# Performance work log

Hardware: AMD Instinct MI355X
Metric: run time of the kernel (lower is better)

The kernel has to match this reference:

```python
import jax, jax.numpy as jnp
import numpy as np

N, C, T, V = 32, 96, 256, 25
S, REL, OUT, BC, KS = 3, 12, 96, 24, 5
DILS = (1, 2)


def setup_inputs() -> dict:
    key = jax.random.key(0)
    ks = jax.random.split(key, 32)
    rn = lambda i, sh, s=1.0: jax.random.normal(ks[i], sh, dtype=jnp.float32) * s
    ru = lambda i, sh: jax.random.uniform(ks[i], sh, dtype=jnp.float32, minval=0.5, maxval=1.5)
    return dict(
        x=rn(0, (N, C, T, V)),
        spd_A=rn(1, (V, V), 0.1),
        A3=rn(2, (S, V, V), 0.1),
        A6=rn(3, (6, V, V), 0.1),
        alpha=jnp.array([0.5], jnp.float32),
        beta=jnp.array([0.5], jnp.float32),
        gamma=jnp.array([0.5], jnp.float32),
        c1_w=rn(4, (S, REL, C), 0.1), c1_b=rn(5, (S, REL), 0.1),
        c2_w=rn(6, (S, REL, C), 0.1), c2_b=rn(7, (S, REL), 0.1),
        c4_w=rn(8, (S, OUT, REL), 0.1), c4_b=rn(9, (S, OUT), 0.1),
        c3_w=rn(10, (S, OUT, C), 0.1), c3_b=rn(11, (S, OUT), 0.1),
        gbn_s=ru(12, (OUT,)), gbn_b=rn(13, (OUT,), 0.1),
        pw_w=rn(14, (4, BC, OUT), 0.1), pw_b=rn(15, (4, BC), 0.1),
        pwbn_s=ru(16, (4, BC)), pwbn_b=rn(17, (4, BC), 0.1),
        tc_w=rn(18, (2, BC, BC, KS), 0.1), tc_b=rn(19, (2, BC), 0.1),
        tcbn_s=ru(20, (2, BC)), tcbn_b=rn(21, (2, BC), 0.1),
        mpbn_s=ru(22, (BC,)), mpbn_b=rn(23, (BC,), 0.1),
    )


def _bn4(h, s, b):  # eval-mode BN folded to per-channel scale/shift, h: [N,C,T,V]
    return h * s[None, :, None, None] + b[None, :, None, None]


def reference(x, spd_A, A3, A6, alpha, beta, gamma,
              c1_w, c1_b, c2_w, c2_b, c4_w, c4_b, c3_w, c3_b,
              gbn_s, gbn_b, pw_w, pw_b, pwbn_s, pwbn_b,
              tc_w, tc_b, tcbn_s, tcbn_b, mpbn_s, mpbn_b):
    # ---- unit_gcn with CTRGC relation modeling ----
    xm = x.mean(axis=2)                                           # [N,C,V] (1x1 conv commutes with T-mean)
    x1 = jnp.einsum('ncv,src->nsrv', xm, c1_w) + c1_b[None, :, :, None]
    x2 = jnp.einsum('ncv,src->nsrv', xm, c2_w) + c2_b[None, :, :, None]
    R = jnp.tanh(x1[..., :, None] - x2[..., None, :])             # [N,S,REL,V,V]
    M = jnp.einsum('nsruv,sor->nsouv', R, c4_w) + c4_b[None, :, :, None, None]
    A6_ex = jnp.tile(A6, (OUT // 6, 1, 1))                        # [OUT,V,V]; A6_ex[c] = A6[c % 6]
    A_at = (M * alpha[0] + A3[None, :, None] + A6_ex[None, None] * beta[0]
            + spd_A * gamma[0])                                   # [N,S,OUT,V,V]
    y = jnp.zeros((N, OUT, T, V), x.dtype)
    for s_ in range(S):
        x3 = jnp.einsum('nctv,oc->notv', x, c3_w[s_]) + c3_b[s_][None, :, None, None]
        y = y + jnp.einsum('nouv,notv->notu', A_at[:, s_], x3)
    y = jax.nn.relu(_bn4(y, gbn_s, gbn_b) + x)                    # residual down = identity (in==out)
    # ---- MultiScale_TemporalConv (internal residual=False) ----
    outs = []
    for b in range(2):  # dilated temporal branches
        h = jax.nn.relu(_bn4(jnp.einsum('nctv,oc->notv', y, pw_w[b])
                             + pw_b[b][None, :, None, None], pwbn_s[b], pwbn_b[b]))
        d = DILS[b]
        pad = 2 * d  # (KS + (KS-1)*(d-1) - 1)//2 for KS=5
        h = jax.lax.conv_general_dilated(
            h, tc_w[b][..., None], window_strides=(1, 1),
            padding=[(pad, pad), (0, 0)], rhs_dilation=(d, 1),
            dimension_numbers=('NCHW', 'OIHW', 'NCHW')) + tc_b[b][None, :, None, None]
        outs.append(_bn4(h, tcbn_s[b], tcbn_b[b]))
    # max-pool branch
    h = jax.nn.relu(_bn4(jnp.einsum('nctv,oc->notv', y, pw_w[2])
                         + pw_b[2][None, :, None, None], pwbn_s[2], pwbn_b[2]))
    h = jax.lax.reduce_window(h, -jnp.inf, jax.lax.max, (1, 1, 3, 1), (1, 1, 1, 1),
                              [(0, 0), (0, 0), (1, 1), (0, 0)])
    outs.append(_bn4(h, mpbn_s, mpbn_b))
    # plain 1x1 branch
    h = jnp.einsum('nctv,oc->notv', y, pw_w[3]) + pw_b[3][None, :, None, None]
    outs.append(_bn4(h, pwbn_s[3], pwbn_b[3]))
    out = jnp.concatenate(outs, axis=1)                           # [N,OUT,T,V]
    return jax.nn.relu(out + x)                                   # outer residual = identity
```

## Files before the change

kernel.cpp:

```cpp
#include <hip/hip_runtime.h>
#include <hip/hip_bf16.h>

typedef __hip_bfloat16 bf16;
typedef __attribute__((ext_vector_type(4))) _Float16 half4;
typedef __attribute__((ext_vector_type(2))) _Float16 half2v;
typedef __attribute__((ext_vector_type(4))) float f32x4;

#define NN 32
#define CC 96
#define TT 256
#define VV 25
#define SS 3
#define RR 12
#define OO 96
#define BCC 24
#define TV (TT*VV)
#define VV2 (VV*VV)

__device__ __forceinline__ float b2f(bf16 v){ return __bfloat162float(v); }
__device__ __forceinline__ bf16  f2b(float v){ return __float2bfloat16(v); }
__device__ __forceinline__ float u2f(unsigned short b){
    union{unsigned u; float f;} a; a.u = ((unsigned)b)<<16; return a.f;
}

__global__ __launch_bounds__(256) void k_mean(const float* __restrict__ x, float* __restrict__ xm)
{
    int idx = blockIdx.x*256 + threadIdx.x;
    if (idx >= NN*CC*VV) return;
    int v  = idx % VV;
    int nc = idx / VV;
    const float* p = x + (size_t)nc*TV + v;
    float s = 0.f;
    for (int t=0;t<TT;t++) s += p[t*VV];
    xm[idx] = s * (1.0f/TT);
}

__global__ __launch_bounds__(256) void k_aat(
    const float* __restrict__ xm,
    const float* __restrict__ c1_w, const float* __restrict__ c1_b,
    const float* __restrict__ c2_w, const float* __restrict__ c2_b,
    const float* __restrict__ c4_w, const float* __restrict__ c4_b,
    const float* __restrict__ A3,  const float* __restrict__ A6, const float* __restrict__ spd,
    const float* __restrict__ alpha, const float* __restrict__ beta, const float* __restrict__ gamma,
    float* __restrict__ Aat)
{
    __shared__ float s_xm[CC*VV];
    __shared__ float s_x1[RR*VV], s_x2[RR*VV];
    __shared__ float s_R[RR*VV2];
    __shared__ float s_c4[OO*RR];
    __shared__ float s_A3[VV2], s_spd[VV2];
    int n = blockIdx.x / SS, s = blockIdx.x % SS;
    int tid = threadIdx.x;
    for (int i=tid;i<CC*VV;i+=256) s_xm[i] = xm[(size_t)n*CC*VV + i];
    for (int i=tid;i<OO*RR;i+=256) s_c4[i] = c4_w[s*OO*RR + i];
    for (int i=tid;i<VV2;i+=256){ s_A3[i]=A3[s*VV2+i]; s_spd[i]=spd[i]; }
    __syncthreads();
    for (int i=tid;i<RR*VV;i+=256){
        int r=i/VV, u=i-r*VV;
        float a1=0.f, a2=0.f;
        for (int c=0;c<CC;c++){
            float xv = s_xm[c*VV+u];
            a1 += c1_w[(s*RR+r)*CC+c]*xv;
            a2 += c2_w[(s*RR+r)*CC+c]*xv;
        }
        s_x1[i]=a1+c1_b[s*RR+r];
        s_x2[i]=a2+c2_b[s*RR+r];
    }
    __syncthreads();
    for (int i=tid;i<RR*VV2;i+=256){
        int r=i/VV2, uv=i-r*VV2, u=uv/VV, v=uv-u*VV;
        s_R[i] = tanhf(s_x1[r*VV+u]-s_x2[r*VV+v]);
    }
    __syncthreads();
    float al=alpha[0], be=beta[0], ga=gamma[0];
    float* op = Aat + ((size_t)n*SS+s)*OO*VV2;
    for (int i=tid;i<OO*VV2;i+=256){
        int o=i/VV2, uv=i-o*VV2;
        float m=0.f;
        #pragma unroll
        for (int r=0;r<RR;r++) m += s_c4[o*RR+r]*s_R[r*VV2+uv];
        m += c4_b[s*OO+o];
        op[i] = m*al + s_A3[uv] + A6[(o%6)*VV2+uv]*be + s_spd[uv]*ga;
    }
}

#define XROW  20
#define X3ROW 84
#define X3OP  (32*X3ROW)
__global__ __launch_bounds__(256,2) void k_gcn(
    const float* __restrict__ x, const float* __restrict__ c3_w, const float* __restrict__ c3_b,
    const float* __restrict__ Aat, const float* __restrict__ gbn_s, const float* __restrict__ gbn_b,
    float* __restrict__ y)
{
    __shared__ __align__(16) _Float16 s_x[800*XROW];
    __shared__ __align__(16) _Float16 s_x3h[4*X3OP];
    __shared__ __align__(16) _Float16 s_w[6*16*16];
    __shared__ float s_cb[16];

    int bi  = blockIdx.x;
    int og  = bi % 24;
    int tcb = (bi/24) & 7;
    int n   = bi / 192;
    int t0  = tcb*32;
    int tid = threadIdx.x;

    for (int i=tid; i<4*32*9; i+=256){
        int op2 = i/288, r2 = i - op2*288;
        int t = r2/9, kk = 75 + (r2 - t*9);
        s_x3h[op2*X3OP + t*X3ROW + kk] = (_Float16)0.f;
    }

    for (int i=tid;i<16*96;i+=256){
        int m=i/96, c=i-m*96;
        float wf = 0.f;
        if (m<12){ int s=m>>2, op=m&3; wf = c3_w[(s*OO + og*4+op)*CC + c]; }
        s_w[((c>>4)*16+m)*16 + (c&15)] = (_Float16)wf;
    }
    if (tid<16){
        float b=0.f;
        if (tid<12){ int s=tid>>2, op=tid&3; b = c3_b[s*OO + og*4+op]; }
        s_cb[tid]=b;
    }

    int l  = tid & 63;
    int li = l & 15, q = l >> 4;
    int wv_id = tid >> 6;
    int o  = og*4 + wv_id;

    half4 areg[2][5];
    #pragma unroll
    for (int mt=0; mt<2; ++mt){
        int u = mt*16 + li;
        #pragma unroll
        for (int kc=0; kc<5; ++kc){
            half4 h;
            #pragma unroll
            for (int e=0; e<4; ++e){
                int k = kc*16 + q*4 + e;
                float av = 0.f;
                if (u < VV && k < 75){
                    int s = k/25, v = k - s*25;
                    av = Aat[(((size_t)n*SS+s)*OO + o)*VV2 + u*VV + v];
                }
                h[e] = (_Float16)av;
            }
            areg[mt][kc] = h;
        }
    }
    float gs = gbn_s[o], gb = gbn_b[o];

    int start = wv_id*13;
    int cnt   = (wv_id<3) ? 13 : 11;

    f32x4 acc[13];
    #pragma unroll
    for (int j=0;j<13;++j) acc[j] = (f32x4){0.f,0.f,0.f,0.f};

    size_t xb = (size_t)n*CC*TV + (size_t)t0*VV;
    for (int ck=0; ck<6; ++ck){
        __syncthreads();
        int c0 = ck*16;
        for (int it=0; it<7; ++it){
            int task = tid + it*256;
            if (task < 1600){
                int cpair = task & 7;
                int pq    = task >> 3;
                const float* r0 = x + xb + (size_t)(c0 + cpair*2)*TV + pq*4;
                float4 a = *(const float4*)r0;
                float4 b = *(const float4*)(r0 + TV);
                #pragma unroll
                for (int ii=0; ii<4; ++ii){
                    int p = pq*4 + ii;
                    half2v hv;
                    hv[0] = (_Float16)((&a.x)[ii]);
                    hv[1] = (_Float16)((&b.x)[ii]);
                    *(half2v*)&s_x[p*XROW + cpair*2] = hv;
                }
            }
        }
        __syncthreads();
        half4 a4 = *(const half4*)(s_w + (ck*16+li)*16 + q*4);
        #pragma unroll
        for (int j=0;j<13;++j){
            if (j < cnt){
                half4 b4 = *(const half4*)(s_x + ((start+j)*16 + li)*XROW + q*4);
                acc[j] = __builtin_amdgcn_mfma_f32_16x16x16f16(a4, b4, acc[j], 0, 0, 0);
            }
        }
    }
    __syncthreads();

    if (q < 3){
        #pragma unroll
        for (int j=0;j<13;++j){
            if (j < cnt){
                int p = (start+j)*16 + li;
                int t = p/25, v = p - t*25;
                int base = t*X3ROW + q*25 + v;
                #pragma unroll
                for (int r=0;r<4;++r)
                    s_x3h[r*X3OP + base] = (_Float16)(acc[j][r] + s_cb[q*4+r]);
            }
        }
    }
    __syncthreads();

    const _Float16* bb = s_x3h + wv_id*X3OP;
    f32x4 acc2[2][2];
    #pragma unroll
    for (int mt=0;mt<2;++mt)
        #pragma unroll
        for (int nt=0;nt<2;++nt) acc2[mt][nt] = (f32x4){0.f,0.f,0.f,0.f};
    #pragma unroll
    for (int kc=0;kc<5;++kc){
        #pragma unroll
        for (int nt=0;nt<2;++nt){
            half4 b4 = *(const half4*)(bb + (nt*16+li)*X3ROW + kc*16 + q*4);
            #pragma unroll
            for (int mt=0;mt<2;++mt)
                acc2[mt][nt] = __builtin_amdgcn_mfma_f32_16x16x16f16(areg[mt][kc], b4, acc2[mt][nt], 0, 0, 0);
        }
    }
    #pragma unroll
    for (int mt=0;mt<2;++mt){
        #pragma unroll
        for (int nt=0;nt<2;++nt){
            int t = nt*16 + li;
            #pragma unroll
            for (int r=0;r<4;++r){
                int u = mt*16 + q*4 + r;
                if (u < VV){
                    size_t oix = ((size_t)(n*OO+o)*TT + (t0+t))*VV + u;
                    float yv = gs*acc2[mt][nt][r] + gb + x[oix];
                    y[oix] = yv>0.f?yv:0.f;
                }
            }
        }
    }
}

__global__ __launch_bounds__(256,2) void k_pw_h(
    const float* __restrict__ yws, const float* __restrict__ pw_w, const float* __restrict__ pw_b,
    const float* __restrict__ pwbn_s, const float* __restrict__ pwbn_b,
    bf16* __restrict__ h1)
{
    __shared__ __align__(16) float s_w[OO*BCC];
    __shared__ float s_sc[BCC], s_sh[BCC];
    int b   = blockIdx.x/160;
    int rem = blockIdx.x - b*160;
    int n   = rem/5;
    int chunk = rem - (rem/5)*5;
    int pbase = chunk*256 + threadIdx.x;
    for (int i=threadIdx.x;i<OO*BCC;i+=256){
        int o=i/BCC, cp=i-o*BCC;
        s_w[i] = pw_w[(b*BCC+cp)*OO + o];
    }
    if (threadIdx.x<BCC){
        int cp=threadIdx.x;
        float sc = pwbn_s[b*BCC+cp];
        s_sc[cp]=sc;
        s_sh[cp]= sc*pw_b[b*BCC+cp] + pwbn_b[b*BCC+cp];
    }
    __syncthreads();
    float acc[5][BCC];
    #pragma unroll
    for (int j=0;j<5;j++)
        #pragma unroll
        for (int i=0;i<BCC;i++) acc[j][i]=0.f;
    const float* yp = yws + (size_t)n*OO*TV + pbase;
    for (int o=0;o<OO;o++){
        float wv[BCC];
        #pragma unroll
        for (int q=0;q<6;q++) *(float4*)&wv[q*4] = *(const float4*)&s_w[o*BCC + q*4];
        float yv[5];
        #pragma unroll
        for (int j=0;j<5;j++) yv[j] = yp[(size_t)o*TV + j*1280];
        #pragma unroll
        for (int j=0;j<5;j++)
            #pragma unroll
            for (int cp=0;cp<BCC;cp++) acc[j][cp] += wv[cp]*yv[j];
    }
    size_t hb = ((size_t)(b*NN+n)*BCC)*TV + pbase;
    #pragma unroll
    for (int j=0;j<5;j++)
        #pragma unroll
        for (int cp=0;cp<BCC;cp++){
            float h = s_sc[cp]*acc[j][cp] + s_sh[cp];
            h1[hb + (size_t)cp*TV + j*1280] = f2b(h>0.f?h:0.f);
        }
}

__global__ __launch_bounds__(256,2) void k_pw3(
    float* yout, const float* __restrict__ pw_w, const float* __restrict__ pw_b,
    const float* __restrict__ pwbn_s, const float* __restrict__ pwbn_b,
    const float* __restrict__ x)
{
    __shared__ __align__(16) float s_w[OO*BCC];
    __shared__ float s_sc[BCC], s_sh[BCC];
    const int b = 3;
    int n   = blockIdx.x/5;
    int chunk = blockIdx.x - n*5;
    int pbase = chunk*256 + threadIdx.x;
    for (int i=threadIdx.x;i<OO*BCC;i+=256){
        int o=i/BCC, cp=i-o*BCC;
        s_w[i] = pw_w[(b*BCC+cp)*OO + o];
    }
    if (threadIdx.x<BCC){
        int cp=threadIdx.x;
        float sc = pwbn_s[b*BCC+cp];
        s_sc[cp]=sc;
        s_sh[cp]= sc*pw_b[b*BCC+cp] + pwbn_b[b*BCC+cp];
    }
    __syncthreads();
    float acc[5][BCC];
    #pragma unroll
    for (int j=0;j<5;j++)
        #pragma unroll
        for (int i=0;i<BCC;i++) acc[j][i]=0.f;
    const float* yp = yout + (size_t)n*OO*TV + pbase;
    for (int o=0;o<OO;o++){
        float wv[BCC];
        #pragma unroll
        for (int q=0;q<6;q++) *(float4*)&wv[q*4] = *(const float4*)&s_w[o*BCC + q*4];
        float yv[5];
        #pragma unroll
        for (int j=0;j<5;j++) yv[j] = yp[(size_t)o*TV + j*1280];
        #pragma unroll
        for (int j=0;j<5;j++)
            #pragma unroll
            for (int cp=0;cp<BCC;cp++) acc[j][cp] += wv[cp]*yv[j];
    }
    size_t ob = ((size_t)n*OO + 72)*TV + pbase;
    #pragma unroll
    for (int j=0;j<5;j++)
        #pragma unroll
        for (int cp=0;cp<BCC;cp++){
            float h = s_sc[cp]*acc[j][cp] + s_sh[cp];
            size_t ix = ob + (size_t)cp*TV + j*1280;
            float r = h + x[ix];
            yout[ix] = r>0.f?r:0.f;
        }
}

template<int D>
__device__ __forceinline__ void tcn_conv(int n, int br, int t0, int t4, int v, int vv, bool act,
    const float* __restrict__ tc_w, const float* __restrict__ tc_b,
    const float* __restrict__ tcbn_s, const float* __restrict__ tcbn_b,
    const float* __restrict__ x, float* __restrict__ out, const unsigned short* s_h)
{
    const int W = 4 + 4*D;
    int tb = 4 + t4*4 - 2*D;
    for (int g=0; g<4; g++){
        float acc[6][4];
        #pragma unroll
        for (int cpi=0;cpi<6;cpi++)
            #pragma unroll
            for (int i=0;i<4;i++) acc[cpi][i]=0.f;
        for (int ci=0; ci<24; ci++){
            float win[W];
            #pragma unroll
            for (int j=0;j<W;j++) win[j] = u2f(s_h[(ci*40 + tb + j)*26 + vv]);
            #pragma unroll
            for (int cpi=0; cpi<6; cpi++){
                int cp = g*6+cpi;
                const float* wp = tc_w + ((br*BCC+cp)*BCC + ci)*5;
                float w0=wp[0],w1=wp[1],w2=wp[2],w3=wp[3],w4=wp[4];
                #pragma unroll
                for (int i=0;i<4;i++)
                    acc[cpi][i] += w0*win[i] + w1*win[i+D] + w2*win[i+2*D]
                                 + w3*win[i+3*D] + w4*win[i+4*D];
            }
        }
        if (act){
            #pragma unroll
            for (int cpi=0; cpi<6; cpi++){
                int ch = br*BCC + g*6+cpi;
                float tbias=tc_b[ch], ts=tcbn_s[ch], tb2=tcbn_b[ch];
                #pragma unroll
                for (int i=0;i<4;i++){
                    size_t oix = ((size_t)(n*OO+ch)*TT + (t0+t4*4+i))*VV + v;
                    float r = ts*(acc[cpi][i]+tbias) + tb2 + x[oix];
                    out[oix] = r>0.f?r:0.f;
                }
            }
        }
    }
}

__global__ __launch_bounds__(256,2) void k_tcn(
    const bf16* __restrict__ h1, const float* __restrict__ tc_w, const float* __restrict__ tc_b,
    const float* __restrict__ tcbn_s, const float* __restrict__ tcbn_b,
    const float* __restrict__ mpbn_s, const float* __restrict__ mpbn_b,
    const float* __restrict__ x, float* __restrict__ out)
{
    __shared__ unsigned short s_h[24*40*26];
    int bi  = blockIdx.x;
    int n   = bi / 24;
    int rem = bi % 24;
    int br  = rem >> 3;
    int tcb = rem & 7;
    int t0  = tcb*32;
    int tid = threadIdx.x;

    const unsigned short* hb = (const unsigned short*)(h1 + ((size_t)(br*NN+n)*BCC)*TV);
    unsigned short padv = (br==2) ? (unsigned short)0xFF80 : (unsigned short)0;
    for (int ci=0; ci<24; ci++){
        const unsigned short* hc = hb + (size_t)ci*TV;
        #pragma unroll
        for (int j=0;j<5;j++){
            int idx = j*256 + tid;
            if (idx < 1040){
                int tt = idx/26, v = idx - tt*26;
                int gt = t0 - 4 + tt;
                unsigned short bits = padv;
                if (v<25 && gt>=0 && gt<TT) bits = hc[gt*VV+v];
                s_h[(ci*40+tt)*26 + v] = bits;
            }
        }
    }
    __syncthreads();

    int t4 = tid>>5, v = tid&31;
    bool act = v<25;
    int vv = act ? v : 24;

    if (br==0){
        tcn_conv<1>(n,br,t0,t4,v,vv,act,tc_w,tc_b,tcbn_s,tcbn_b,x,out,s_h);
    } else if (br==1){
        tcn_conv<2>(n,br,t0,t4,v,vv,act,tc_w,tc_b,tcbn_s,tcbn_b,x,out,s_h);
    } else {
        int tb = 4 + t4*4 - 1;
        for (int cp=0; cp<24; cp++){
            float win[6];
            #pragma unroll
            for (int j=0;j<6;j++) win[j] = u2f(s_h[(cp*40 + tb + j)*26 + vv]);
            float ms=mpbn_s[cp], mb=mpbn_b[cp];
            if (act){
                #pragma unroll
                for (int i=0;i<4;i++){
                    float m = fmaxf(fmaxf(win[i],win[i+1]),win[i+2]);
                    size_t oix = ((size_t)(n*OO+(48+cp))*TT + (t0+t4*4+i))*VV + v;
                    float r = ms*m + mb + x[oix];
                    out[oix] = r>0.f?r:0.f;
                }
            }
        }
    }
}

extern "C" void kernel_launch(void* const* d_in, const int* in_sizes, int n_in,
                              void* d_out, int out_size, void* d_ws, size_t ws_size,
                              hipStream_t stream)
{
    const float* x     = (const float*)d_in[0];
    const float* spd   = (const float*)d_in[1];
    const float* A3    = (const float*)d_in[2];
    const float* A6    = (const float*)d_in[3];
    const float* alpha = (const float*)d_in[4];
    const float* beta  = (const float*)d_in[5];
    const float* gamma = (const float*)d_in[6];
    const float* c1_w  = (const float*)d_in[7];
    const float* c1_b  = (const float*)d_in[8];
    const float* c2_w  = (const float*)d_in[9];
    const float* c2_b  = (const float*)d_in[10];
    const float* c4_w  = (const float*)d_in[11];
    const float* c4_b  = (const float*)d_in[12];
    const float* c3_w  = (const float*)d_in[13];
    const float* c3_b  = (const float*)d_in[14];
    const float* gbn_s = (const float*)d_in[15];
    const float* gbn_b = (const float*)d_in[16];
    const float* pw_w  = (const float*)d_in[17];
    const float* pw_b  = (const float*)d_in[18];
    const float* pwbn_s= (const float*)d_in[19];
    const float* pwbn_b= (const float*)d_in[20];
    const float* tc_w  = (const float*)d_in[21];
    const float* tc_b  = (const float*)d_in[22];
    const float* tcbn_s= (const float*)d_in[23];
    const float* tcbn_b= (const float*)d_in[24];
    const float* mpbn_s= (const float*)d_in[25];
    const float* mpbn_b= (const float*)d_in[26];
    float* out = (float*)d_out;

    char* ws = (char*)d_ws;
    float* xm  = (float*)(ws);
    float* Aat = (float*)(ws + 307200);
    bf16*  h1  = (bf16*)(ws);

    k_mean<<<dim3(300), dim3(256), 0, stream>>>(x, xm);
    k_aat <<<dim3(96),  dim3(256), 0, stream>>>(xm, c1_w,c1_b,c2_w,c2_b,c4_w,c4_b,
                                                A3, A6, spd, alpha, beta, gamma, Aat);
    k_gcn <<<dim3(6144),dim3(256), 0, stream>>>(x, c3_w, c3_b, Aat, gbn_s, gbn_b, out);
    k_pw_h<<<dim3(480), dim3(256), 0, stream>>>(out, pw_w, pw_b, pwbn_s, pwbn_b, h1);
    k_pw3 <<<dim3(160), dim3(256), 0, stream>>>(out, pw_w, pw_b, pwbn_s, pwbn_b, x);
    k_tcn <<<dim3(768), dim3(256), 0, stream>>>(h1, tc_w, tc_b, tcbn_s, tcbn_b,
                                                mpbn_s, mpbn_b, x, out);
}
```

Before: 809.5 us.

## Load x and conv weights directly into MFMA registers, dropping LDS staging

The k_gcn kernel no longer stages the x tile and c3 weights through shared memory. Each lane now loads its MFMA B operands straight from global memory as scalar strided reads and converts them to fp16. The A operands come from float4 weight loads, and the bias is read directly. This removes the shared-memory buffers and the per-chunk barriers, and it raises launch_bounds occupancy from 2 to 4 blocks. The cost is uncoalesced scalar global loads (a stride of TV between channels, 16 apart per j), which may hurt memory efficiency.

```diff
diff --git a/kernel.cpp b/kernel.cpp
--- a/kernel.cpp
+++ b/kernel.cpp
@@ -84,18 +84,14 @@
     }
 }
 
-#define XROW  20
 #define X3ROW 84
 #define X3OP  (32*X3ROW)
-__global__ __launch_bounds__(256,2) void k_gcn(
+__global__ __launch_bounds__(256,4) void k_gcn(
     const float* __restrict__ x, const float* __restrict__ c3_w, const float* __restrict__ c3_b,
     const float* __restrict__ Aat, const float* __restrict__ gbn_s, const float* __restrict__ gbn_b,
     float* __restrict__ y)
 {
-    __shared__ __align__(16) _Float16 s_x[800*XROW];
     __shared__ __align__(16) _Float16 s_x3h[4*X3OP];
-    __shared__ __align__(16) _Float16 s_w[6*16*16];
-    __shared__ float s_cb[16];
 
     int bi  = blockIdx.x;
     int og  = bi % 24;
@@ -108,18 +104,6 @@
         int op2 = i/288, r2 = i - op2*288;
         int t = r2/9, kk = 75 + (r2 - t*9);
         s_x3h[op2*X3OP + t*X3ROW + kk] = (_Float16)0.f;
-    }
-
-    for (int i=tid;i<16*96;i+=256){
-        int m=i/96, c=i-m*96;
-        float wf = 0.f;
-        if (m<12){ int s=m>>2, op=m&3; wf = c3_w[(s*OO + og*4+op)*CC + c]; }
-        s_w[((c>>4)*16+m)*16 + (c&15)] = (_Float16)wf;
-    }
-    if (tid<16){
-        float b=0.f;
-        if (tid<12){ int s=tid>>2, op=tid&3; b = c3_b[s*OO + og*4+op]; }
-        s_cb[tid]=b;
     }
 
     int l  = tid & 63;
@@ -157,39 +141,37 @@
     for (int j=0;j<13;++j) acc[j] = (f32x4){0.f,0.f,0.f,0.f};
 
     size_t xb = (size_t)n*CC*TV + (size_t)t0*VV;
+    bool wok = (li < 12);
+    int  wrow = wok ? ((li>>2)*OO + og*4 + (li&3)) : 0;
+    const float* wp  = c3_w + (size_t)wrow*CC + q*4;
+    const float* xpb = x + xb + (size_t)(q*4)*TV + start*16 + li;
+
     for (int ck=0; ck<6; ++ck){
-        __syncthreads();
-        int c0 = ck*16;
-        for (int it=0; it<7; ++it){
-            int task = tid + it*256;
-            if (task < 1600){
-                int cpair = task & 7;
-                int pq    = task >> 3;
-                const float* r0 = x + xb + (size_t)(c0 + cpair*2)*TV + pq*4;
-                float4 a = *(const float4*)r0;
-                float4 b = *(const float4*)(r0 + TV);
-                #pragma unroll
-                for (int ii=0; ii<4; ++ii){
-                    int p = pq*4 + ii;
-                    half2v hv;
-                    hv[0] = (_Float16)((&a.x)[ii]);
-                    hv[1] = (_Float16)((&b.x)[ii]);
-                    *(half2v*)&s_x[p*XROW + cpair*2] = hv;
-                }
-            }
-        }
-        __syncthreads();
-        half4 a4 = *(const half4*)(s_w + (ck*16+li)*16 + q*4);
+        float4 wv4 = *(const float4*)(wp + ck*16);
+        half4 a4;
+        a4[0] = (_Float16)(wok ? wv4.x : 0.f);
+        a4[1] = (_Float16)(wok ? wv4.y : 0.f);
+        a4[2] = (_Float16)(wok ? wv4.z : 0.f);
+        a4[3] = (_Float16)(wok ? wv4.w : 0.f);
+        const float* xc0 = xpb + (size_t)(ck*16)*TV;
+        const float* xc1 = xc0 + TV;
+        const float* xc2 = xc1 + TV;
+        const float* xc3 = xc2 + TV;
         #pragma unroll
         for (int j=0;j<13;++j){
             if (j < cnt){
-                half4 b4 = *(const half4*)(s_x + ((start+j)*16 + li)*XROW + q*4);
+                half4 b4;
+                b4[0] = (_Float16)xc0[j*16];
+                b4[1] = (_Float16)xc1[j*16];
+                b4[2] = (_Float16)xc2[j*16];
+                b4[3] = (_Float16)xc3[j*16];
                 acc[j] = __builtin_amdgcn_mfma_f32_16x16x16f16(a4, b4, acc[j], 0, 0, 0);
             }
         }
     }
-    __syncthreads();
-
+
+    int qq = (q<3) ? q : 0;
+    float4 cb4 = *(const float4*)(c3_b + qq*OO + og*4);
     if (q < 3){
         #pragma unroll
         for (int j=0;j<13;++j){
@@ -197,9 +179,10 @@
                 int p = (start+j)*16 + li;
                 int t = p/25, v = p - t*25;
                 int base = t*X3ROW + q*25 + v;
-                #pragma unroll
-                for (int r=0;r<4;++r)
-                    s_x3h[r*X3OP + base] = (_Float16)(acc[j][r] + s_cb[q*4+r]);
+                s_x3h[0*X3OP + base] = (_Float16)(acc[j][0] + cb4.x);
+                s_x3h[1*X3OP + base] = (_Float16)(acc[j][1] + cb4.y);
+                s_x3h[2*X3OP + base] = (_Float16)(acc[j][2] + cb4.z);
+                s_x3h[3*X3OP + base] = (_Float16)(acc[j][3] + cb4.w);
             }
         }
     }
```

Result: faster. 684.5 us (-15.4%).
